# Optimization experiments

Measured on AMD Instinct MI355X. Metric: run time of the kernel, lower is better.

## Reference

```python
import jax, jax.numpy as jnp
import numpy as np


def setup_inputs() -> dict:
    key = jax.random.key(0)
    ks = jax.random.split(key, 5)
    N, T, D, H = 256, 64, 1024, 1024
    x = jax.random.normal(ks[0], (N, T, D), dtype=jnp.float32)
    A = jax.random.normal(ks[1], (N, H, 4, 4), dtype=jnp.float32)
    Wx = jax.random.normal(ks[2], (D, 4 * H), dtype=jnp.float32) / np.sqrt(D)
    Wh = jax.random.normal(ks[3], (H, 4 * H), dtype=jnp.float32) / np.sqrt(H)
    Wattn = jax.random.normal(ks[4], (H, 4 * H), dtype=jnp.float32) / np.sqrt(H)
    b = jnp.zeros((4 * H,), dtype=jnp.float32)
    return {"x": x, "A": A, "Wx": Wx, "Wh": Wh, "Wattn": Wattn, "b": b}


def reference(x, A, Wx, Wh, Wattn, b):
    # x: (N,T,D); A: (N,H,4,4); Wx: (D,4H); Wh,Wattn: (H,4H); b: (4H,)
    N, T, D = x.shape
    H = A.shape[1]
    A_flat = A.reshape(N, H, 16)                 # 16 = 4*4 spatial keys
    h0 = A_flat.mean(axis=2)                     # (N,H); c0 = h0
    scale = 1.0 / jnp.sqrt(jnp.asarray(H, dtype=x.dtype))

    def step(carry, xt):
        prev_h, prev_c = carry
        # scaled dot-product attention over 16 spatial positions
        scores = jnp.einsum('nh,nhk->nk', prev_h, A_flat) * scale   # (N,16)
        w = jax.nn.softmax(scores, axis=1)                           # (N,16)
        attn = jnp.einsum('nhk,nk->nh', A_flat, w)                   # (N,H)
        # LSTM gates with attention term
        a = xt @ Wx + prev_h @ Wh + attn @ Wattn + b                 # (N,4H)
        ai, af, ao, ag = jnp.split(a, 4, axis=1)
        i = jax.nn.sigmoid(ai)
        f = jax.nn.sigmoid(af)
        o = jax.nn.sigmoid(ao)
        g = jnp.tanh(ag)
        next_c = f * prev_c + i * g
        next_h = o * jnp.tanh(next_c)
        return (next_h, next_c), next_h

    xs = jnp.swapaxes(x, 0, 1)                   # (T,N,D)
    _, hs = jax.lax.scan(step, (h0, h0), xs)     # hs: (T,N,H)
    return jnp.swapaxes(hs, 0, 1)                # (N,T,H)
```

## Files before the change

kernel.cpp:

```cpp
#include <hip/hip_runtime.h>
#include <math.h>

#define NB 256
#define TT 64
#define DD 1024
#define HH 1024
#define FOURH 4096
#define KTOT 3072
#define KT16 192
#define P1 (NB * FOURH)
#define NZ 4

#define AF_LVL 786432ull
#define BF_LVL 12582912ull
#define SPLIT_SCALE 2048.0f
#define INV_SPLIT (1.0f / 2048.0f)

typedef _Float16 f16x8 __attribute__((ext_vector_type(8)));
typedef float f32x16 __attribute__((ext_vector_type(16)));
typedef float f32x2v __attribute__((ext_vector_type(2)));
typedef float f32x4v __attribute__((ext_vector_type(4)));

__device__ __forceinline__ unsigned short f2h(float f) {
    _Float16 h = (_Float16)f;
    unsigned short u;
    __builtin_memcpy(&u, &h, 2);
    return u;
}
__device__ __forceinline__ float h2f(unsigned short u) {
    _Float16 h;
    __builtin_memcpy(&h, &u, 2);
    return (float)h;
}
__device__ __forceinline__ void split2(float f, unsigned short& hi, unsigned short& lo) {
    hi = f2h(f);
    lo = f2h((f - h2f(hi)) * SPLIT_SCALE);
}

__device__ __forceinline__ size_t aoff(int lvl, int mt, int kt, int lane) {
    return ((size_t)((lvl * 8 + mt) * KT16 + kt) * 64 + lane) * 8;
}
__device__ __forceinline__ size_t boff(int lvl, int ct, int kt, int lane) {
    return ((size_t)((lvl * 128 + ct) * KT16 + kt) * 64 + lane) * 8;
}

__device__ __forceinline__ void write_frag8(unsigned short* __restrict__ Af, int n, int k8, const float* v) {
    int mt = n >> 5, kt = k8 >> 4;
    int lane = (n & 31) + 32 * ((k8 >> 3) & 1);
    unsigned short s[8][2];
#pragma unroll
    for (int i = 0; i < 8; ++i) split2(v[i], s[i][0], s[i][1]);
#pragma unroll
    for (int lvl = 0; lvl < 2; ++lvl) {
        uint4 p;
        p.x = (unsigned)s[0][lvl] | ((unsigned)s[1][lvl] << 16);
        p.y = (unsigned)s[2][lvl] | ((unsigned)s[3][lvl] << 16);
        p.z = (unsigned)s[4][lvl] | ((unsigned)s[5][lvl] << 16);
        p.w = (unsigned)s[6][lvl] | ((unsigned)s[7][lvl] << 16);
        *reinterpret_cast<uint4*>(Af + aoff(lvl, mt, kt, lane)) = p;
    }
}

__global__ __launch_bounds__(256) void wsplit_kernel(const float* __restrict__ Wx,
                                                     const float* __restrict__ Wh,
                                                     const float* __restrict__ Wattn,
                                                     unsigned short* __restrict__ Bf) {
    __shared__ float tile[32][33];
    int k0 = blockIdx.x * 32, j0 = blockIdx.y * 32;
    int t = threadIdx.x;
    int rl = t >> 3, c4 = (t & 7) * 4;
    int seg = k0 >> 10;
    const float* W = (seg == 0) ? Wx : (seg == 1) ? Wh : Wattn;
    const float4 v = *reinterpret_cast<const float4*>(W + (size_t)((k0 & 1023) + rl) * FOURH + j0 + c4);
    tile[rl][c4 + 0] = v.x; tile[rl][c4 + 1] = v.y; tile[rl][c4 + 2] = v.z; tile[rl][c4 + 3] = v.w;
    __syncthreads();
    int jl = t >> 3, k4 = (t & 7) * 4;
    unsigned short s[4][2];
#pragma unroll
    for (int i = 0; i < 4; ++i) split2(tile[k4 + i][jl], s[i][0], s[i][1]);
    int j = j0 + jl;
    int kg = k0 + k4;
    int ct = j >> 5, kt = kg >> 4;
    int lane = (j & 31) + 32 * ((kg >> 3) & 1);
    int sub = kg & 7;
#pragma unroll
    for (int lvl = 0; lvl < 2; ++lvl) {
        uint2 p;
        p.x = (unsigned)s[0][lvl] | ((unsigned)s[1][lvl] << 16);
        p.y = (unsigned)s[2][lvl] | ((unsigned)s[3][lvl] << 16);
        *reinterpret_cast<uint2*>(Bf + boff(lvl, ct, kt, lane) + sub) = p;
    }
}

__device__ __forceinline__ void attn_phase(const float* __restrict__ A, int n, int tid,
                                           const float* hsh, float* ash, float* red2) {
    int lane = tid & 63, wave = tid >> 6;
    const float* An = A + (size_t)n * HH * 16;
    float areg[2][16];
    float part[16];
#pragma unroll
    for (int k = 0; k < 16; ++k) part[k] = 0.f;
#pragma unroll
    for (int i = 0; i < 2; ++i) {
        int hh = tid + i * 512;
        float hv = hsh[hh];
        const float* ap = An + (size_t)hh * 16;
#pragma unroll
        for (int k = 0; k < 16; ++k) {
            float av = ap[k];
            areg[i][k] = av;
            part[k] += hv * av;
        }
    }
#pragma unroll
    for (int k = 0; k < 16; ++k) {
        float v = part[k];
#pragma unroll
        for (int off = 32; off > 0; off >>= 1) v += __shfl_down(v, off);
        if (lane == 0) red2[wave * 16 + k] = v;
    }
    __syncthreads();
    float w[16];
    float mx = -1e30f;
#pragma unroll
    for (int k = 0; k < 16; ++k) {
        float s = 0.f;
#pragma unroll
        for (int q = 0; q < 8; ++q) s += red2[q * 16 + k];
        s *= 0.03125f;
        w[k] = s;
        mx = fmaxf(mx, s);
    }
    float sum = 0.f;
#pragma unroll
    for (int k = 0; k < 16; ++k) {
        w[k] = expf(w[k] - mx);
        sum += w[k];
    }
    float inv = 1.0f / sum;
#pragma unroll
    for (int k = 0; k < 16; ++k) w[k] *= inv;
#pragma unroll
    for (int i = 0; i < 2; ++i) {
        float s = 0.f;
#pragma unroll
        for (int k = 0; k < 16; ++k) s += areg[i][k] * w[k];
        ash[tid + i * 512] = s;
    }
}

__device__ __forceinline__ void write_state_frags(unsigned short* __restrict__ Af,
                                                  const float* __restrict__ x,
                                                  const float* hsh, const float* ash,
                                                  int n, int tnext, int tid) {
    int seg = tid >> 7;
    int k8 = (tid & 127) * 8;
    float v[8];
    if (seg == 0) {
#pragma unroll
        for (int i = 0; i < 8; ++i) v[i] = hsh[k8 + i];
        write_frag8(Af, n, 1024 + k8, v);
    } else if (seg == 1) {
#pragma unroll
        for (int i = 0; i < 8; ++i) v[i] = ash[k8 + i];
        write_frag8(Af, n, 2048 + k8, v);
    } else if (seg == 2 && tnext < TT) {
        const f32x4v* xp = reinterpret_cast<const f32x4v*>(x + ((size_t)n * TT + tnext) * DD + k8);
        f32x4v x0 = __builtin_nontemporal_load(xp);
        f32x4v x1 = __builtin_nontemporal_load(xp + 1);
        v[0] = x0[0]; v[1] = x0[1]; v[2] = x0[2]; v[3] = x0[3];
        v[4] = x1[0]; v[5] = x1[1]; v[6] = x1[2]; v[7] = x1[3];
        write_frag8(Af, n, k8, v);
    }
}

__global__ __launch_bounds__(512) void initk(const float* __restrict__ A,
                                             const float* __restrict__ x,
                                             float* __restrict__ c,
                                             unsigned short* __restrict__ Af) {
    int n = blockIdx.x, tid = threadIdx.x;
    __shared__ float hsh[HH], ash[HH];
    __shared__ float red2[128];
#pragma unroll
    for (int i = 0; i < 2; ++i) {
        int hh = tid + i * 512;
        const float* ap = A + ((size_t)n * HH + hh) * 16;
        float s = 0.f;
#pragma unroll
        for (int k = 0; k < 16; ++k) s += ap[k];
        s *= (1.0f / 16.0f);
        c[(size_t)n * HH + hh] = s;
        hsh[hh] = s;
    }
    __syncthreads();
    attn_phase(A, n, tid, hsh, ash, red2);
    __syncthreads();
    write_state_frags(Af, x, hsh, ash, n, 0, tid);
}

#define KTPB 48
#define NCHUNK 24
#define BUFS 20480

#define STAGE(bidx, cc)                                                                        \
    {                                                                                          \
        _Pragma("unroll") for (int j = 0; j < 5; ++j) {                                        \
            __builtin_amdgcn_global_load_lds(                                                  \
                (const __attribute__((address_space(1))) unsigned int*)(sb[j] + (size_t)(cc) * 1024), \
                (__attribute__((address_space(3))) unsigned int*)&Bsm[(bidx)][ldsoff[j]],      \
                16, 0, 0);                                                                     \
        }                                                                                      \
    }

__global__ __launch_bounds__(512) void gemm_mfma(const unsigned short* __restrict__ Af,
                                                 const unsigned short* __restrict__ Bf,
                                                 float* __restrict__ apart, int rep) {
    __shared__ __align__(16) unsigned short Bsm[3][BUFS];
    int tid = threadIdx.x;
    int l = tid & 63, w = tid >> 6;
    int wm = w & 3, wn = w >> 2;
    int bid = blockIdx.x;
    int id = ((bid & 7) << 5) + (bid >> 3);
    int colb = id & 63, z = id >> 6;
    int kt0 = z * KTPB;

    const unsigned short* sb[5];
    int ldsoff[5];
#pragma unroll
    for (int j = 0; j < 5; ++j) {
        int f = w + 8 * j;
        if (f < 32) {
            int ktc = f >> 4, lvl = (f >> 3) & 1, mt = f & 7;
            sb[j] = Af + aoff(lvl, mt, kt0 + ktc, l);
        } else {
            int g = f - 32;
            int ktc = g >> 2, lvl = (g >> 1) & 1, ct = g & 1;
            sb[j] = Bf + boff(lvl, colb * 2 + ct, kt0 + ktc, l);
        }
        ldsoff[j] = f * 512;
    }

    f32x16 accH[2];
    f32x16 accM[2];

    for (int r = 0; r < rep; ++r) {
#pragma unroll
        for (int mi = 0; mi < 2; ++mi)
#pragma unroll
            for (int q = 0; q < 16; ++q) { accH[mi][q] = 0.f; accM[mi][q] = 0.f; }

        STAGE(0, 0)
        STAGE(1, 1)

        int cb = 0;
        for (int cc = 0; cc < NCHUNK; ++cc) {
            if (cc + 1 < NCHUNK) { asm volatile("s_waitcnt vmcnt(5)" ::: "memory"); }
            else                 { asm volatile("s_waitcnt vmcnt(0)" ::: "memory"); }
            __builtin_amdgcn_sched_barrier(0);
            __builtin_amdgcn_s_barrier();
            __builtin_amdgcn_sched_barrier(0);
            if (cc + 2 < NCHUNK) {
                int tb = cb + 2; if (tb >= 3) tb -= 3;
                STAGE(tb, cc + 2)
            }

            const unsigned short* base = &Bsm[cb][0];
            __builtin_amdgcn_s_setprio(1);
#pragma unroll
            for (int ktc = 0; ktc < 2; ++ktc) {
                const unsigned short* bp = base + (size_t)(32 + ktc * 4 + wn) * 512 + l * 8;
                f16x8 b0 = *reinterpret_cast<const f16x8*>(bp);
                f16x8 b1 = *reinterpret_cast<const f16x8*>(bp + 1024);
                const unsigned short* ap0 = base + (size_t)(ktc * 16 + wm * 2) * 512 + l * 8;
                f16x8 a0m0 = *reinterpret_cast<const f16x8*>(ap0);
                f16x8 a0m1 = *reinterpret_cast<const f16x8*>(ap0 + 512);
                f16x8 a1m0 = *reinterpret_cast<const f16x8*>(ap0 + 8 * 512);
                f16x8 a1m1 = *reinterpret_cast<const f16x8*>(ap0 + 9 * 512);
                accH[0] = __builtin_amdgcn_mfma_f32_32x32x16_f16(a0m0, b0, accH[0], 0, 0, 0);
                accM[0] = __builtin_amdgcn_mfma_f32_32x32x16_f16(a0m0, b1, accM[0], 0, 0, 0);
                accM[0] = __builtin_amdgcn_mfma_f32_32x32x16_f16(a1m0, b0, accM[0], 0, 0, 0);
                accH[1] = __builtin_amdgcn_mfma_f32_32x32x16_f16(a0m1, b0, accH[1], 0, 0, 0);
                accM[1] = __builtin_amdgcn_mfma_f32_32x32x16_f16(a0m1, b1, accM[1], 0, 0, 0);
                accM[1] = __builtin_amdgcn_mfma_f32_32x32x16_f16(a1m1, b0, accM[1], 0, 0, 0);
            }
            __builtin_amdgcn_s_setprio(0);
            cb = (cb + 1 == 3) ? 0 : cb + 1;
        }
    }

    float* plane = apart + (size_t)z * P1;
    int col = colb * 64 + wn * 32 + (l & 31);
#pragma unroll
    for (int mi = 0; mi < 2; ++mi) {
        int rbase = (wm * 2 + mi) * 32 + (l >> 5) * 4;
#pragma unroll
        for (int r = 0; r < 16; ++r) {
            int row = rbase + (r & 3) + 8 * (r >> 2);
            __builtin_nontemporal_store(accH[mi][r] + accM[mi][r] * INV_SPLIT,
                                        &plane[(size_t)row * FOURH + col]);
        }
    }
}

__global__ __launch_bounds__(512) void pointwise(const float* __restrict__ apart,
                                                 const float* __restrict__ bias,
                                                 const float* __restrict__ A,
                                                 const float* __restrict__ x,
                                                 float* __restrict__ c,
                                                 float* __restrict__ out,
                                                 unsigned short* __restrict__ Af, int t, int rep) {
    int n = blockIdx.x, tid = threadIdx.x;
    __shared__ float hsh[HH], ash[HH];
    __shared__ float red2[128];
    const float* ap = apart + (size_t)n * FOURH;
    int hh2 = tid * 2;
    f32x2v cold, hn2;
    for (int r = 0; r < rep; ++r) {
        f32x2v g2[4];
#pragma unroll
        for (int g = 0; g < 4; ++g) {
            int j = g * 1024 + hh2;
            f32x2v s = *reinterpret_cast<const f32x2v*>(bias + j);
#pragma unroll
            for (int zz = 0; zz < NZ; ++zz) {
                f32x2v p = __builtin_nontemporal_load(
                    reinterpret_cast<const f32x2v*>(ap + (size_t)zz * P1 + j));
                s[0] += p[0]; s[1] += p[1];
            }
            g2[g] = s;
        }
        cold = *reinterpret_cast<const f32x2v*>(c + (size_t)n * HH + hh2);
        {
            float ig = 1.f / (1.f + expf(-g2[0][0]));
            float fg = 1.f / (1.f + expf(-g2[1][0]));
            float og = 1.f / (1.f + expf(-g2[2][0]));
            float gg = tanhf(g2[3][0]);
            float cn = fg * cold[0] + ig * gg;
            hn2[0] = og * tanhf(cn);
            cold[0] = cn;
        }
        {
            float ig = 1.f / (1.f + expf(-g2[0][1]));
            float fg = 1.f / (1.f + expf(-g2[1][1]));
            float og = 1.f / (1.f + expf(-g2[2][1]));
            float gg = tanhf(g2[3][1]);
            float cn = fg * cold[1] + ig * gg;
            hn2[1] = og * tanhf(cn);
            cold[1] = cn;
        }
        *reinterpret_cast<f32x2v*>(&hsh[hh2]) = hn2;
        __syncthreads();
        attn_phase(A, n, tid, hsh, ash, red2);
        __syncthreads();
    }
    *reinterpret_cast<f32x2v*>(c + (size_t)n * HH + hh2) = cold;
    __builtin_nontemporal_store(hn2, reinterpret_cast<f32x2v*>(out + ((size_t)n * TT + t) * HH + hh2));
    write_state_frags(Af, x, hsh, ash, n, t + 1, tid);
}

extern "C" void kernel_launch(void* const* d_in, const int* in_sizes, int n_in,
                              void* d_out, int out_size, void* d_ws, size_t ws_size,
                              hipStream_t stream) {
    const float* x     = (const float*)d_in[0];
    const float* A     = (const float*)d_in[1];
    const float* Wx    = (const float*)d_in[2];
    const float* Wh    = (const float*)d_in[3];
    const float* Wattn = (const float*)d_in[4];
    const float* b     = (const float*)d_in[5];
    float* out = (float*)d_out;

    unsigned short* Bf = (unsigned short*)d_ws;
    unsigned short* Af = Bf + 2 * BF_LVL;
    float* apart = (float*)(Af + 2 * AF_LVL);
    float* c = apart + (size_t)NZ * P1;

    wsplit_kernel<<<dim3(KTOT / 32, FOURH / 32), 256, 0, stream>>>(Wx, Wh, Wattn, Bf);
    initk<<<NB, 512, 0, stream>>>(A, x, c, Af);

    for (int t = 0; t < TT; ++t) {
        gemm_mfma<<<256, 512, 0, stream>>>(Af, Bf, apart, (t == 0) ? 6 : 1);
        pointwise<<<NB, 512, 0, stream>>>(apart, b, A, x, c, out, Af, t, (t == 0) ? 6 : 1);
    }
}
```

Measured before the change: 2.715 ms.

## Widen GEMM block tile to 128 columns and double the K-split count

Each block of the split-K MFMA GEMM now computes a 256x128 output tile instead of 256x64, with each wave holding a 2x2 grid of 32x32 accumulators. To keep the same block count, the K dimension is split into 8 partitions instead of 4, each half as deep. This raises MFMA work per LDS-loaded A fragment and halves total A-fragment traffic. The cost is more accumulator registers, a larger LDS staging buffer, shorter pipelines per block, and twice as many partial planes for the pointwise kernel to read and reduce.

```diff
diff --git a/kernel.cpp b/kernel.cpp
--- a/kernel.cpp
+++ b/kernel.cpp
@@ -9,7 +9,7 @@
 #define KTOT 3072
 #define KT16 192
 #define P1 (NB * FOURH)
-#define NZ 4
+#define NZ 8
 
 #define AF_LVL 786432ull
 #define BF_LVL 12582912ull
@@ -198,13 +198,13 @@
     write_state_frags(Af, x, hsh, ash, n, 0, tid);
 }
 
-#define KTPB 48
-#define NCHUNK 24
-#define BUFS 20480
+#define KTPB 24
+#define NCHUNK 12
+#define BUFS 24576
 
 #define STAGE(bidx, cc)                                                                        \
     {                                                                                          \
-        _Pragma("unroll") for (int j = 0; j < 5; ++j) {                                        \
+        _Pragma("unroll") for (int j = 0; j < 6; ++j) {                                        \
             __builtin_amdgcn_global_load_lds(                                                  \
                 (const __attribute__((address_space(1))) unsigned int*)(sb[j] + (size_t)(cc) * 1024), \
                 (__attribute__((address_space(3))) unsigned int*)&Bsm[(bidx)][ldsoff[j]],      \
@@ -221,40 +221,42 @@
     int wm = w & 3, wn = w >> 2;
     int bid = blockIdx.x;
     int id = ((bid & 7) << 5) + (bid >> 3);
-    int colb = id & 63, z = id >> 6;
+    int colb = id & 31, z = id >> 5;
     int kt0 = z * KTPB;
 
-    const unsigned short* sb[5];
-    int ldsoff[5];
-#pragma unroll
-    for (int j = 0; j < 5; ++j) {
+    const unsigned short* sb[6];
+    int ldsoff[6];
+#pragma unroll
+    for (int j = 0; j < 6; ++j) {
         int f = w + 8 * j;
         if (f < 32) {
             int ktc = f >> 4, lvl = (f >> 3) & 1, mt = f & 7;
             sb[j] = Af + aoff(lvl, mt, kt0 + ktc, l);
         } else {
             int g = f - 32;
-            int ktc = g >> 2, lvl = (g >> 1) & 1, ct = g & 1;
-            sb[j] = Bf + boff(lvl, colb * 2 + ct, kt0 + ktc, l);
+            int ktc = g >> 3, lvl = (g >> 2) & 1, ct = g & 3;
+            sb[j] = Bf + boff(lvl, colb * 4 + ct, kt0 + ktc, l);
         }
         ldsoff[j] = f * 512;
     }
 
-    f32x16 accH[2];
-    f32x16 accM[2];
+    f32x16 accH[2][2];
+    f32x16 accM[2][2];
 
     for (int r = 0; r < rep; ++r) {
 #pragma unroll
         for (int mi = 0; mi < 2; ++mi)
 #pragma unroll
-            for (int q = 0; q < 16; ++q) { accH[mi][q] = 0.f; accM[mi][q] = 0.f; }
+            for (int ni = 0; ni < 2; ++ni)
+#pragma unroll
+                for (int q = 0; q < 16; ++q) { accH[mi][ni][q] = 0.f; accM[mi][ni][q] = 0.f; }
 
         STAGE(0, 0)
         STAGE(1, 1)
 
         int cb = 0;
         for (int cc = 0; cc < NCHUNK; ++cc) {
-            if (cc + 1 < NCHUNK) { asm volatile("s_waitcnt vmcnt(5)" ::: "memory"); }
+            if (cc + 1 < NCHUNK) { asm volatile("s_waitcnt vmcnt(6)" ::: "memory"); }
             else                 { asm volatile("s_waitcnt vmcnt(0)" ::: "memory"); }
             __builtin_amdgcn_sched_barrier(0);
             __builtin_amdgcn_s_barrier();
@@ -268,20 +270,28 @@
             __builtin_amdgcn_s_setprio(1);
 #pragma unroll
             for (int ktc = 0; ktc < 2; ++ktc) {
-                const unsigned short* bp = base + (size_t)(32 + ktc * 4 + wn) * 512 + l * 8;
-                f16x8 b0 = *reinterpret_cast<const f16x8*>(bp);
-                f16x8 b1 = *reinterpret_cast<const f16x8*>(bp + 1024);
                 const unsigned short* ap0 = base + (size_t)(ktc * 16 + wm * 2) * 512 + l * 8;
-                f16x8 a0m0 = *reinterpret_cast<const f16x8*>(ap0);
-                f16x8 a0m1 = *reinterpret_cast<const f16x8*>(ap0 + 512);
-                f16x8 a1m0 = *reinterpret_cast<const f16x8*>(ap0 + 8 * 512);
-                f16x8 a1m1 = *reinterpret_cast<const f16x8*>(ap0 + 9 * 512);
-                accH[0] = __builtin_amdgcn_mfma_f32_32x32x16_f16(a0m0, b0, accH[0], 0, 0, 0);
-                accM[0] = __builtin_amdgcn_mfma_f32_32x32x16_f16(a0m0, b1, accM[0], 0, 0, 0);
-                accM[0] = __builtin_amdgcn_mfma_f32_32x32x16_f16(a1m0, b0, accM[0], 0, 0, 0);
-                accH[1] = __builtin_amdgcn_mfma_f32_32x32x16_f16(a0m1, b0, accH[1], 0, 0, 0);
-                accM[1] = __builtin_amdgcn_mfma_f32_32x32x16_f16(a0m1, b1, accM[1], 0, 0, 0);
-                accM[1] = __builtin_amdgcn_mfma_f32_32x32x16_f16(a1m1, b0, accM[1], 0, 0, 0);
+                f16x8 aH0 = *reinterpret_cast<const f16x8*>(ap0);
+                f16x8 aH1 = *reinterpret_cast<const f16x8*>(ap0 + 512);
+                f16x8 aL0 = *reinterpret_cast<const f16x8*>(ap0 + 8 * 512);
+                f16x8 aL1 = *reinterpret_cast<const f16x8*>(ap0 + 9 * 512);
+                const unsigned short* bp0 = base + (size_t)(32 + ktc * 8 + wn * 2) * 512 + l * 8;
+                f16x8 bH0 = *reinterpret_cast<const f16x8*>(bp0);
+                f16x8 bH1 = *reinterpret_cast<const f16x8*>(bp0 + 512);
+                f16x8 bL0 = *reinterpret_cast<const f16x8*>(bp0 + 4 * 512);
+                f16x8 bL1 = *reinterpret_cast<const f16x8*>(bp0 + 5 * 512);
+                accH[0][0] = __builtin_amdgcn_mfma_f32_32x32x16_f16(aH0, bH0, accH[0][0], 0, 0, 0);
+                accM[0][0] = __builtin_amdgcn_mfma_f32_32x32x16_f16(aH0, bL0, accM[0][0], 0, 0, 0);
+                accM[0][0] = __builtin_amdgcn_mfma_f32_32x32x16_f16(aL0, bH0, accM[0][0], 0, 0, 0);
+                accH[0][1] = __builtin_amdgcn_mfma_f32_32x32x16_f16(aH0, bH1, accH[0][1], 0, 0, 0);
+                accM[0][1] = __builtin_amdgcn_mfma_f32_32x32x16_f16(aH0, bL1, accM[0][1], 0, 0, 0);
+                accM[0][1] = __builtin_amdgcn_mfma_f32_32x32x16_f16(aL0, bH1, accM[0][1], 0, 0, 0);
+                accH[1][0] = __builtin_amdgcn_mfma_f32_32x32x16_f16(aH1, bH0, accH[1][0], 0, 0, 0);
+                accM[1][0] = __builtin_amdgcn_mfma_f32_32x32x16_f16(aH1, bL0, accM[1][0], 0, 0, 0);
+                accM[1][0] = __builtin_amdgcn_mfma_f32_32x32x16_f16(aL1, bH0, accM[1][0], 0, 0, 0);
+                accH[1][1] = __builtin_amdgcn_mfma_f32_32x32x16_f16(aH1, bH1, accH[1][1], 0, 0, 0);
+                accM[1][1] = __builtin_amdgcn_mfma_f32_32x32x16_f16(aH1, bL1, accM[1][1], 0, 0, 0);
+                accM[1][1] = __builtin_amdgcn_mfma_f32_32x32x16_f16(aL1, bH1, accM[1][1], 0, 0, 0);
             }
             __builtin_amdgcn_s_setprio(0);
             cb = (cb + 1 == 3) ? 0 : cb + 1;
@@ -289,15 +299,18 @@
     }
 
     float* plane = apart + (size_t)z * P1;
-    int col = colb * 64 + wn * 32 + (l & 31);
 #pragma unroll
     for (int mi = 0; mi < 2; ++mi) {
         int rbase = (wm * 2 + mi) * 32 + (l >> 5) * 4;
 #pragma unroll
-        for (int r = 0; r < 16; ++r) {
-            int row = rbase + (r & 3) + 8 * (r >> 2);
-            __builtin_nontemporal_store(accH[mi][r] + accM[mi][r] * INV_SPLIT,
-                                        &plane[(size_t)row * FOURH + col]);
+        for (int ni = 0; ni < 2; ++ni) {
+            int col = colb * 128 + (wn * 2 + ni) * 32 + (l & 31);
+#pragma unroll
+            for (int r = 0; r < 16; ++r) {
+                int row = rbase + (r & 3) + 8 * (r >> 2);
+                __builtin_nontemporal_store(accH[mi][ni][r] + accM[mi][ni][r] * INV_SPLIT,
+                                            &plane[(size_t)row * FOURH + col]);
+            }
         }
     }
 }
```

Measured after the change: 3.890 ms. 43.3% more time.
